# Kernel optimization log

Measured on AMD Instinct MI355X. Metric: run time of the kernel, lower is better.

Reference implementation:

```python
import jax, jax.numpy as jnp
import numpy as np

N, E, G = 10000, 160000, 64
F, C1, C2, C3, K, NC = 128, 128, 256, 512, 5, 10


def setup_inputs() -> dict:
    key = jax.random.key(0)
    ks = jax.random.split(key, 12)
    s = 0.05
    return {
        "x": jax.random.normal(ks[0], (N, F), dtype=jnp.float32),
        "edge_index": jax.random.randint(ks[1], (2, E), 0, N, dtype=jnp.int64),
        "batch": jnp.sort(jax.random.randint(ks[2], (N,), 0, G, dtype=jnp.int64)),
        "W_cheb": jax.random.normal(ks[3], (K, F, C1), dtype=jnp.float32) * s,
        "b_cheb": jnp.zeros((C1,), jnp.float32),
        "W_g1": jax.random.normal(ks[4], (C1, C2), dtype=jnp.float32) * s,
        "b_g1": jnp.zeros((C2,), jnp.float32),
        "W_g2": jax.random.normal(ks[5], (C2, C3), dtype=jnp.float32) * s,
        "b_g2": jnp.zeros((C3,), jnp.float32),
        "w_gate": jax.random.normal(ks[6], (C3, 1), dtype=jnp.float32) * s,
        "b_gate": jnp.zeros((1,), jnp.float32),
        "W_fc": jax.random.normal(ks[7], (C3, NC), dtype=jnp.float32) * s,
        "b_fc": jnp.zeros((NC,), jnp.float32),
    }


def _deg_inv_sqrt(deg):
    return jnp.where(deg > 0, jax.lax.rsqrt(jnp.maximum(deg, 1e-12)), 0.0)


def cheb_conv(x, src, dst, W, b):
    # PyG ChebConv, sym normalization, lambda_max=2 => scaled Laplacian = -D^-1/2 A D^-1/2
    ones = jnp.ones((src.shape[0],), x.dtype)
    deg = jax.ops.segment_sum(ones, src, num_segments=N)
    dinv = _deg_inv_sqrt(deg)
    w = -(dinv[src] * dinv[dst])  # [E]

    def prop(h):
        return jax.ops.segment_sum(w[:, None] * h[src], dst, num_segments=N)

    tx0 = x
    tx1 = prop(x)
    out = tx0 @ W[0] + tx1 @ W[1]
    for k in range(2, W.shape[0]):
        tx2 = 2.0 * prop(tx1) - tx0
        out = out + tx2 @ W[k]
        tx0, tx1 = tx1, tx2
    return out + b


def gcn_conv(x, src, dst, W, b):
    # PyG GCNConv: add self-loops, sym norm D~^-1/2 (A+I) D~^-1/2, transform then aggregate
    loop = jnp.arange(N, dtype=src.dtype)
    src_a = jnp.concatenate([src, loop])
    dst_a = jnp.concatenate([dst, loop])
    ones = jnp.ones((src_a.shape[0],), x.dtype)
    deg = jax.ops.segment_sum(ones, dst_a, num_segments=N)
    dinv = _deg_inv_sqrt(deg)
    norm = dinv[src_a] * dinv[dst_a]  # [E+N]
    h = x @ W
    return jax.ops.segment_sum(norm[:, None] * h[src_a], dst_a, num_segments=N) + b


def attention_pool(x, batch, w_gate, b_gate):
    logits = (x @ w_gate + b_gate)[:, 0]  # [N]
    m = jax.ops.segment_max(logits, batch, num_segments=G)
    e = jnp.exp(logits - m[batch])
    s = jax.ops.segment_sum(e, batch, num_segments=G)
    alpha = e / s[batch]
    return jax.ops.segment_sum(alpha[:, None] * x, batch, num_segments=G)  # [G, C3]


def reference(x, edge_index, batch, W_cheb, b_cheb, W_g1, b_g1, W_g2, b_g2,
              w_gate, b_gate, W_fc, b_fc):
    src, dst = edge_index[0], edge_index[1]
    h = jax.nn.relu(cheb_conv(x, src, dst, W_cheb, b_cheb))
    h = jax.nn.relu(gcn_conv(h, src, dst, W_g1, b_g1))
    h = jax.nn.relu(gcn_conv(h, src, dst, W_g2, b_g2))
    g = attention_pool(h, batch, w_gate, b_gate)
    logits = g @ W_fc + b_fc
    return jax.nn.log_softmax(logits, axis=1)
```

## Files before the change

### kernel.cpp

```cpp
#include <hip/hip_runtime.h>
#include <hip/hip_bf16.h>
#include <math.h>

#define N_NODES 10000
#define N_EDGES 160000
#define N_GRAPHS 64
#define F_IN    128
#define C1_DIM  128
#define C2_DIM  256
#define C3_DIM  512
#define K_CHEB  5
#define NCLS    10
#define TC      (K_CHEB * F_IN)

typedef short v8s __attribute__((ext_vector_type(8)));
typedef float v4f __attribute__((ext_vector_type(4)));

static __device__ __forceinline__ unsigned short f2bf(float f) {
    unsigned u = __float_as_uint(f);
    unsigned r = (u + 0x7FFFu + ((u >> 16) & 1u)) >> 16;
    return (unsigned short)r;
}
static __device__ __forceinline__ float bf_lo(unsigned u) { return __uint_as_float(u << 16); }
static __device__ __forceinline__ float bf_hi(unsigned u) { return __uint_as_float(u & 0xFFFF0000u); }

#define PREP_A (N_NODES * 32)
#define PREP_B (TC * C1_DIM)
#define PREP_C (C1_DIM * C2_DIM)
#define PREP_D (C2_DIM * C3_DIM)
#define PREP_E N_NODES
#define PREP_F N_NODES
#define PREP_H (N_GRAPHS * C3_DIM)
#define PREP_G N_EDGES
#define PREP_TOTAL (PREP_A + PREP_B + PREP_C + PREP_D + PREP_E + PREP_F + PREP_H + PREP_G)
__global__ void prep_kernel(const float* __restrict__ x, unsigned short* __restrict__ tcat,
                            const float* __restrict__ Wcheb, unsigned short* __restrict__ Wcb_t,
                            const float* __restrict__ Wg1, unsigned short* __restrict__ Wg1_t,
                            const float* __restrict__ Wg2, unsigned short* __restrict__ Wg2_t,
                            const int* __restrict__ batch, int* __restrict__ gptr,
                            float* __restrict__ logits, float* __restrict__ pooled,
                            const int* __restrict__ src, const int* __restrict__ dst,
                            int* __restrict__ cnt_s, int* __restrict__ cnt_d) {
    int id = blockIdx.x * blockDim.x + threadIdx.x;
    if (id < PREP_A) {
        int n = id >> 5, f = (id & 31) * 4;
        float4 v = *(const float4*)(x + (size_t)n * F_IN + f);
        ushort4 o; o.x = f2bf(v.x); o.y = f2bf(v.y); o.z = f2bf(v.z); o.w = f2bf(v.w);
        *(ushort4*)(tcat + (size_t)n * TC + f) = o;
        return;
    }
    id -= PREP_A;
    if (id < PREP_B) {
        int k = id % TC, n = id / TC;
        Wcb_t[(size_t)n * TC + k] = f2bf(Wcheb[(size_t)k * C1_DIM + n]);
        return;
    }
    id -= PREP_B;
    if (id < PREP_C) {
        int k = id % C1_DIM, n = id / C1_DIM;
        Wg1_t[(size_t)n * C1_DIM + k] = f2bf(Wg1[(size_t)k * C2_DIM + n]);
        return;
    }
    id -= PREP_C;
    if (id < PREP_D) {
        int k = id % C2_DIM, n = id / C2_DIM;
        Wg2_t[(size_t)n * C2_DIM + k] = f2bf(Wg2[(size_t)k * C3_DIM + n]);
        return;
    }
    id -= PREP_D;
    if (id < PREP_E) {
        int i = id;
        int b = batch[i];
        if (i == 0) { for (int g = 0; g <= b; g++) gptr[g] = 0; }
        else {
            int bp = batch[i - 1];
            for (int g = bp + 1; g <= b; g++) gptr[g] = i;
        }
        if (i == N_NODES - 1) { for (int g = b + 1; g <= N_GRAPHS; g++) gptr[g] = N_NODES; }
        return;
    }
    id -= PREP_E;
    if (id < PREP_F) { logits[id] = 0.0f; return; }
    id -= PREP_F;
    if (id < PREP_H) { pooled[id] = 0.0f; return; }
    id -= PREP_H;
    if (id < PREP_G) {
        atomicAdd(&cnt_s[src[id]], 1);
        atomicAdd(&cnt_d[dst[id]], 1);
    }
}

__global__ __launch_bounds__(256) void fill_scan_kernel(
        const int* __restrict__ src, const int* __restrict__ dst,
        const int* __restrict__ cnt_s, const int* __restrict__ cnt_d,
        int* __restrict__ rowptr, int* __restrict__ fillc,
        int2* __restrict__ ecb, int2* __restrict__ egc, int E, int n) {
    __shared__ int ldsc[N_NODES];
    __shared__ int sums[256];
    int tid = threadIdx.x;
    for (int i = tid; i < n; i += 256) ldsc[i] = cnt_d[i];
    __syncthreads();
    int chunk = (n + 255) / 256;
    int s0 = min(n, tid * chunk), s1 = min(n, s0 + chunk);
    int loc = 0;
    for (int i = s0; i < s1; i++) loc += ldsc[i];
    sums[tid] = loc;
    __syncthreads();
    for (int off = 1; off < 256; off <<= 1) {
        int t = (tid >= off) ? sums[tid - off] : 0;
        __syncthreads();
        sums[tid] += t;
        __syncthreads();
    }
    int pre = sums[tid] - loc;
    for (int i = s0; i < s1; i++) { int v = ldsc[i]; ldsc[i] = pre; pre += v; }
    __syncthreads();
    if (blockIdx.x == 0) {
        for (int i = tid; i < n; i += 256) rowptr[i] = ldsc[i];
        if (tid == 255) rowptr[n] = pre;
    }
    int e = blockIdx.x * 256 + tid;
    if (e >= E) return;
    int s = src[e], d = dst[e];
    int pos = ldsc[d] + atomicAdd(&fillc[d], 1);
    int cs = cnt_s[s], cd = cnt_s[d];
    float ds = (cs > 0) ? rsqrtf((float)cs) : 0.0f;
    float dd = (cd > 0) ? rsqrtf((float)cd) : 0.0f;
    float nr = rsqrtf((float)cnt_d[s] + 1.0f) * rsqrtf((float)cnt_d[d] + 1.0f);
    ecb[pos] = make_int2(s, __float_as_int(-(ds * dd)));
    egc[pos] = make_int2(s, __float_as_int(nr));
}

__global__ __launch_bounds__(256) void gather_cheb_bf(
        const unsigned short* __restrict__ tb, const int* __restrict__ rowptr,
        const int2* __restrict__ edges,
        const unsigned short* __restrict__ base, float alpha, float beta,
        unsigned short* __restrict__ outc, int n) {
    int w = (blockIdx.x * blockDim.x + threadIdx.x) >> 6;
    int lane = threadIdx.x & 63;
    if (w >= n) return;
    w = __builtin_amdgcn_readfirstlane(w);
    int rs = __builtin_amdgcn_readfirstlane(rowptr[w]);
    int re = __builtin_amdgcn_readfirstlane(rowptr[w + 1]);
    float a0 = 0.0f, a1 = 0.0f;
    for (int b = rs; b < re; b += 64) {
        int nv = min(64, re - b);
        int cl = 0, wlb = 0;
        if (b + lane < re) { int2 e = edges[b + lane]; cl = e.x; wlb = e.y; }
        int nk = (nv + 15) & ~15;
        for (int j = 0; j < nk; j += 16) {
            int ss[16]; float ww[16]; unsigned uu[16];
            #pragma unroll
            for (int q = 0; q < 16; q++) {
                ss[q] = __builtin_amdgcn_readlane(cl, j + q);
                ww[q] = __uint_as_float((unsigned)__builtin_amdgcn_readlane(wlb, j + q));
            }
            #pragma unroll
            for (int q = 0; q < 16; q++)
                uu[q] = *(const unsigned*)(tb + (size_t)ss[q] * TC + lane * 2);
            #pragma unroll
            for (int q = 0; q < 16; q++) { a0 += ww[q] * bf_lo(uu[q]); a1 += ww[q] * bf_hi(uu[q]); }
        }
    }
    if (base) {
        unsigned ub = ((const unsigned*)(base + (size_t)w * TC))[lane];
        a0 = alpha * a0 + beta * bf_lo(ub);
        a1 = alpha * a1 + beta * bf_hi(ub);
    } else {
        a0 *= alpha; a1 *= alpha;
    }
    ushort2 o; o.x = f2bf(a0); o.y = f2bf(a1);
    *(ushort2*)(outc + (size_t)w * TC + lane * 2) = o;
}

template<int FPL>
__global__ __launch_bounds__(256) void gather_gcn_pre(
        const unsigned short* __restrict__ tb, const int* __restrict__ rowptr,
        const int2* __restrict__ edges,
        const int* __restrict__ cnt_d, unsigned short* __restrict__ z, int n) {
    const int C = FPL * 64;
    int w = (blockIdx.x * blockDim.x + threadIdx.x) >> 6;
    int lane = threadIdx.x & 63;
    if (w >= n) return;
    w = __builtin_amdgcn_readfirstlane(w);
    int rs = __builtin_amdgcn_readfirstlane(rowptr[w]);
    int re = __builtin_amdgcn_readfirstlane(rowptr[w + 1]);
    float acc[FPL];
    #pragma unroll
    for (int q = 0; q < FPL; q++) acc[q] = 0.0f;
    for (int b = rs; b < re; b += 64) {
        int nv = min(64, re - b);
        int cl = 0, wlb = 0;
        if (b + lane < re) { int2 e = edges[b + lane]; cl = e.x; wlb = e.y; }
        int nk = (nv + 15) & ~15;
        for (int j = 0; j < nk; j += 16) {
            int ss[16]; float ww[16];
            #pragma unroll
            for (int q = 0; q < 16; q++) {
                ss[q] = __builtin_amdgcn_readlane(cl, j + q);
                ww[q] = __uint_as_float((unsigned)__builtin_amdgcn_readlane(wlb, j + q));
            }
            if constexpr (FPL == 2) {
                unsigned uu[16];
                #pragma unroll
                for (int q = 0; q < 16; q++)
                    uu[q] = *(const unsigned*)(tb + (size_t)ss[q] * C + lane * 2);
                #pragma unroll
                for (int q = 0; q < 16; q++) { acc[0] += ww[q] * bf_lo(uu[q]); acc[1] += ww[q] * bf_hi(uu[q]); }
            } else {
                uint2 uu[16];
                #pragma unroll
                for (int q = 0; q < 16; q++)
                    uu[q] = *(const uint2*)(tb + (size_t)ss[q] * C + lane * 4);
                #pragma unroll
                for (int q = 0; q < 16; q++) {
                    acc[0] += ww[q] * bf_lo(uu[q].x); acc[1] += ww[q] * bf_hi(uu[q].x);
                    acc[2] += ww[q] * bf_lo(uu[q].y); acc[3] += ww[q] * bf_hi(uu[q].y);
                }
            }
        }
    }
    float sn = 1.0f / (float)(cnt_d[w] + 1);
    if constexpr (FPL == 2) {
        unsigned u = ((const unsigned*)(tb + (size_t)w * C))[lane];
        acc[0] += sn * bf_lo(u); acc[1] += sn * bf_hi(u);
        ushort2 o; o.x = f2bf(acc[0]); o.y = f2bf(acc[1]);
        *(ushort2*)(z + (size_t)w * C + lane * 2) = o;
    } else {
        uint2 u = ((const uint2*)(tb + (size_t)w * C))[lane];
        acc[0] += sn * bf_lo(u.x); acc[1] += sn * bf_hi(u.x);
        acc[2] += sn * bf_lo(u.y); acc[3] += sn * bf_hi(u.y);
        ushort4 o; o.x = f2bf(acc[0]); o.y = f2bf(acc[1]);
        o.z = f2bf(acc[2]); o.w = f2bf(acc[3]);
        *(ushort4*)(z + (size_t)w * C + lane * 4) = o;
    }
}

template<int JT, int KC>
__global__ __launch_bounds__(256) void gemm_bf16(
        const unsigned short* __restrict__ A, const unsigned short* __restrict__ Bt,
        const float* __restrict__ bias,
        unsigned short* __restrict__ Cb, const float* __restrict__ wg,
        float* __restrict__ logits, int M, int N) {
    int m0 = blockIdx.y * 64, n0 = blockIdx.x * (JT * 32);
    int wave = threadIdx.x >> 6, lane = threadIdx.x & 63;
    int wm = (wave & 1) * 32, wn = (wave >> 1) * (JT * 16);
    int l15 = lane & 15, quad = lane >> 4;

    v4f acc[2][JT];
    #pragma unroll
    for (int i = 0; i < 2; i++)
        #pragma unroll
        for (int j = 0; j < JT; j++) acc[i][j] = (v4f){0.f, 0.f, 0.f, 0.f};

    const unsigned short* Ab[2]; bool av[2];
    #pragma unroll
    for (int i = 0; i < 2; i++) {
        int row = m0 + wm + i * 16 + l15;
        av[i] = row < M;
        Ab[i] = A + (size_t)(av[i] ? row : 0) * KC + quad * 8;
    }
    const unsigned short* Bb[JT];
    #pragma unroll
    for (int j = 0; j < JT; j++) {
        int coln = n0 + wn + j * 16 + l15;
        Bb[j] = Bt + (size_t)coln * KC + quad * 8;
    }
    const v8s zero8 = {0, 0, 0, 0, 0, 0, 0, 0};

    #pragma unroll
    for (int k0 = 0; k0 < KC; k0 += 32) {
        v8s a[2], b[JT];
        #pragma unroll
        for (int i = 0; i < 2; i++) a[i] = av[i] ? *(const v8s*)(Ab[i] + k0) : zero8;
        #pragma unroll
        for (int j = 0; j < JT; j++) b[j] = *(const v8s*)(Bb[j] + k0);
        #pragma unroll
        for (int i = 0; i < 2; i++)
            #pragma unroll
            for (int j = 0; j < JT; j++)
                acc[i][j] = __builtin_amdgcn_mfma_f32_16x16x32_bf16(a[i], b[j], acc[i][j], 0, 0, 0);
    }

    float bv[JT], wgj[JT];
    #pragma unroll
    for (int j = 0; j < JT; j++) {
        int coln = n0 + wn + j * 16 + l15;
        bv[j] = bias[coln];
        wgj[j] = wg ? wg[coln] : 0.0f;
    }
    #pragma unroll
    for (int i = 0; i < 2; i++) {
        #pragma unroll
        for (int r = 0; r < 4; r++) {
            int row = m0 + wm + i * 16 + quad * 4 + r;
            if (row >= M) continue;
            float gval = 0.0f;
            #pragma unroll
            for (int j = 0; j < JT; j++) {
                int coln = n0 + wn + j * 16 + l15;
                float v = fmaxf(acc[i][j][r] + bv[j], 0.0f);
                Cb[(size_t)row * N + coln] = f2bf(v);
                gval += v * wgj[j];
            }
            if (wg) {
                #pragma unroll
                for (int off = 1; off < 16; off <<= 1) gval += __shfl_xor(gval, off);
                if (l15 == 0) atomicAdd(&logits[row], gval);
            }
        }
    }
}

__global__ __launch_bounds__(256) void pool_partial(const unsigned short* __restrict__ h3b,
        const float* __restrict__ logits, const int* __restrict__ gptr,
        float* __restrict__ pooled) {
    __shared__ float red[256];
    int g = blockIdx.x, sl = blockIdx.y, tid = threadIdx.x;
    int gs = gptr[g], ge = gptr[g + 1];
    float m = -INFINITY;
    for (int i = gs + tid; i < ge; i += 256) m = fmaxf(m, logits[i]);
    red[tid] = m; __syncthreads();
    for (int off = 128; off > 0; off >>= 1) {
        if (tid < off) red[tid] = fmaxf(red[tid], red[tid + off]);
        __syncthreads();
    }
    m = red[0]; __syncthreads();
    float s = 0.0f;
    for (int i = gs + tid; i < ge; i += 256) s += expf(logits[i] - m);
    red[tid] = s; __syncthreads();
    for (int off = 128; off > 0; off >>= 1) {
        if (tid < off) red[tid] += red[tid + off];
        __syncthreads();
    }
    s = red[0];
    float sinv = (s > 0.0f) ? 1.0f / s : 0.0f;
    int cnt = ge - gs;
    int i0 = gs + (cnt * sl) / 8;
    int i1 = gs + (cnt * (sl + 1)) / 8;
    float a0 = 0.0f, a1 = 0.0f;
    for (int i = i0; i < i1; i++) {
        float al = expf(logits[i] - m) * sinv;
        unsigned u = ((const unsigned*)(h3b + (size_t)i * C3_DIM))[tid];
        a0 += al * bf_lo(u);
        a1 += al * bf_hi(u);
    }
    if (i1 > i0) {
        atomicAdd(&pooled[(size_t)g * C3_DIM + tid * 2 + 0], a0);
        atomicAdd(&pooled[(size_t)g * C3_DIM + tid * 2 + 1], a1);
    }
}

__global__ void fc_kernel(const float* __restrict__ pooled, const float* __restrict__ Wfc,
                          const float* __restrict__ bfc, float* __restrict__ out) {
    int g = blockIdx.x;
    int t = threadIdx.x;
    float acc = -INFINITY;
    if (t < NCLS) {
        acc = bfc[t];
        for (int k = 0; k < C3_DIM; k++)
            acc += pooled[(size_t)g * C3_DIM + k] * Wfc[k * NCLS + t];
    }
    float m = acc;
    #pragma unroll
    for (int off = 8; off > 0; off >>= 1) m = fmaxf(m, __shfl_xor(m, off, 16));
    float e = (t < NCLS) ? expf(acc - m) : 0.0f;
    float s = e;
    #pragma unroll
    for (int off = 8; off > 0; off >>= 1) s += __shfl_xor(s, off, 16);
    if (t < NCLS) out[g * NCLS + t] = acc - m - logf(s);
}

extern "C" void kernel_launch(void* const* d_in, const int* in_sizes, int n_in,
                              void* d_out, int out_size, void* d_ws, size_t ws_size,
                              hipStream_t stream) {
    const float* x      = (const float*)d_in[0];
    const int*   ei     = (const int*)d_in[1];
    const int*   batch  = (const int*)d_in[2];
    const float* W_cheb = (const float*)d_in[3];
    const float* b_cheb = (const float*)d_in[4];
    const float* W_g1   = (const float*)d_in[5];
    const float* b_g1   = (const float*)d_in[6];
    const float* W_g2   = (const float*)d_in[7];
    const float* b_g2   = (const float*)d_in[8];
    const float* w_gate = (const float*)d_in[9];
    const float* W_fc   = (const float*)d_in[11];
    const float* b_fc   = (const float*)d_in[12];
    const int* src = ei;
    const int* dst = ei + N_EDGES;
    float* out = (float*)d_out;

    const int N = N_NODES, E = N_EDGES, G = N_GRAPHS;

    char* Wp = (char*)d_ws;
    auto alloc = [&](size_t bytes) {
        void* p = Wp;
        Wp += (bytes + 255) & ~(size_t)255;
        return p;
    };
    int*   cnt3    = (int*)alloc((size_t)3 * N * 4);
    int*   cnt_s   = cnt3;
    int*   cnt_d   = cnt3 + N;
    int*   fillc   = cnt3 + 2 * N;
    int*   rowptr  = (int*)alloc((N + 1) * 4);
    int2*  ecb     = (int2*)alloc((size_t)E * 8);
    int2*  egc     = (int2*)alloc((size_t)E * 8);
    unsigned short* tcat  = (unsigned short*)alloc((size_t)N * TC * 2);
    unsigned short* h1b   = (unsigned short*)alloc((size_t)N * C1_DIM * 2);
    unsigned short* z1b   = (unsigned short*)alloc((size_t)N * C1_DIM * 2);
    unsigned short* h2b   = (unsigned short*)alloc((size_t)N * C2_DIM * 2);
    unsigned short* z2b   = (unsigned short*)alloc((size_t)N * C2_DIM * 2);
    unsigned short* h3b   = (unsigned short*)alloc((size_t)N * C3_DIM * 2);
    unsigned short* Wcb_t = (unsigned short*)alloc((size_t)TC * C1_DIM * 2);
    unsigned short* Wg1_t = (unsigned short*)alloc((size_t)C1_DIM * C2_DIM * 2);
    unsigned short* Wg2_t = (unsigned short*)alloc((size_t)C2_DIM * C3_DIM * 2);
    float* logits  = (float*)alloc(N * 4);
    int*   gptr    = (int*)alloc((G + 1) * 4);
    float* pooled  = (float*)alloc((size_t)G * C3_DIM * 4);

    dim3 blk(256);
    auto cdiv = [](int a, int b) { return (a + b - 1) / b; };

    hipMemsetAsync(cnt3, 0, (size_t)3 * N * sizeof(int), stream);
    hipLaunchKernelGGL(prep_kernel, dim3(cdiv(PREP_TOTAL, 256)), blk, 0, stream,
                       x, tcat, W_cheb, Wcb_t, W_g1, Wg1_t, W_g2, Wg2_t,
                       batch, gptr, logits, pooled, src, dst, cnt_s, cnt_d);

    hipLaunchKernelGGL(fill_scan_kernel, dim3(cdiv(E, 256)), blk, 0, stream,
                       src, dst, cnt_s, cnt_d, rowptr, fillc, ecb, egc, E, N);

    const int NWB = cdiv(N, 4);

    hipLaunchKernelGGL(gather_cheb_bf, dim3(NWB), blk, 0, stream,
                       tcat + 0 * F_IN, rowptr, ecb,
                       (const unsigned short*)nullptr, 1.0f, 0.0f, tcat + 1 * F_IN, N);
    hipLaunchKernelGGL(gather_cheb_bf, dim3(NWB), blk, 0, stream,
                       tcat + 1 * F_IN, rowptr, ecb,
                       tcat + 0 * F_IN, 2.0f, -1.0f, tcat + 2 * F_IN, N);
    hipLaunchKernelGGL(gather_cheb_bf, dim3(NWB), blk, 0, stream,
                       tcat + 2 * F_IN, rowptr, ecb,
                       tcat + 1 * F_IN, 2.0f, -1.0f, tcat + 3 * F_IN, N);
    hipLaunchKernelGGL(gather_cheb_bf, dim3(NWB), blk, 0, stream,
                       tcat + 3 * F_IN, rowptr, ecb,
                       tcat + 2 * F_IN, 2.0f, -1.0f, tcat + 4 * F_IN, N);

    hipLaunchKernelGGL((gemm_bf16<2, TC>), dim3(C1_DIM / 64, cdiv(N, 64)), blk, 0, stream,
                       tcat, Wcb_t, b_cheb, h1b,
                       (const float*)nullptr, (float*)nullptr, N, C1_DIM);

    hipLaunchKernelGGL(gather_gcn_pre<2>, dim3(NWB), blk, 0, stream,
                       h1b, rowptr, egc, cnt_d, z1b, N);
    hipLaunchKernelGGL((gemm_bf16<4, C1_DIM>), dim3(C2_DIM / 128, cdiv(N, 64)), blk, 0, stream,
                       z1b, Wg1_t, b_g1, h2b,
                       (const float*)nullptr, (float*)nullptr, N, C2_DIM);

    hipLaunchKernelGGL(gather_gcn_pre<4>, dim3(NWB), blk, 0, stream,
                       h2b, rowptr, egc, cnt_d, z2b, N);
    hipLaunchKernelGGL((gemm_bf16<4, C2_DIM>), dim3(C3_DIM / 128, cdiv(N, 64)), blk, 0, stream,
                       z2b, Wg2_t, b_g2, h3b,
                       w_gate, logits, N, C3_DIM);

    hipLaunchKernelGGL(pool_partial, dim3(G, 8), blk, 0, stream, h3b, logits, gptr, pooled);
    hipLaunchKernelGGL(fc_kernel, dim3(G), dim3(64), 0, stream, pooled, W_fc, b_fc, out);
}
```

Before: 259.7 us.

## Fuse gather, GEMM, pool and FC stages into one cooperative persistent kernel

Replaces the ten separate stage kernels (four Chebyshev gathers, three GEMMs, two GCN gathers, pool, FC) with a single cooperative mega-kernel. The grid is sized from occupancy and capped at 1024 blocks, each stage uses grid-stride loops, and grid.sync() separates the stages. The aim is to remove per-launch overhead and inter-kernel gaps. In exchange it adds grid-wide barriers, caps parallelism to resident blocks, and may raise register pressure because all stage code lives in one kernel.

```diff
diff --git a/kernel.cpp b/kernel.cpp
--- a/kernel.cpp
+++ b/kernel.cpp
@@ -1,6 +1,9 @@
 #include <hip/hip_runtime.h>
+#include <hip/hip_cooperative_groups.h>
 #include <hip/hip_bf16.h>
 #include <math.h>
+
+namespace cg = cooperative_groups;
 
 #define N_NODES 10000
 #define N_EDGES 160000
@@ -131,244 +134,303 @@
     egc[pos] = make_int2(s, __float_as_int(nr));
 }
 
-__global__ __launch_bounds__(256) void gather_cheb_bf(
+static __device__ void dev_gather_cheb(
         const unsigned short* __restrict__ tb, const int* __restrict__ rowptr,
         const int2* __restrict__ edges,
         const unsigned short* __restrict__ base, float alpha, float beta,
-        unsigned short* __restrict__ outc, int n) {
-    int w = (blockIdx.x * blockDim.x + threadIdx.x) >> 6;
-    int lane = threadIdx.x & 63;
-    if (w >= n) return;
-    w = __builtin_amdgcn_readfirstlane(w);
-    int rs = __builtin_amdgcn_readfirstlane(rowptr[w]);
-    int re = __builtin_amdgcn_readfirstlane(rowptr[w + 1]);
-    float a0 = 0.0f, a1 = 0.0f;
-    for (int b = rs; b < re; b += 64) {
-        int nv = min(64, re - b);
-        int cl = 0, wlb = 0;
-        if (b + lane < re) { int2 e = edges[b + lane]; cl = e.x; wlb = e.y; }
-        int nk = (nv + 15) & ~15;
-        for (int j = 0; j < nk; j += 16) {
-            int ss[16]; float ww[16]; unsigned uu[16];
-            #pragma unroll
-            for (int q = 0; q < 16; q++) {
-                ss[q] = __builtin_amdgcn_readlane(cl, j + q);
-                ww[q] = __uint_as_float((unsigned)__builtin_amdgcn_readlane(wlb, j + q));
+        unsigned short* __restrict__ outc, int n, int wave0, int nwaves, int lane) {
+    for (int w0 = wave0; w0 < n; w0 += nwaves) {
+        int w = __builtin_amdgcn_readfirstlane(w0);
+        int rs = __builtin_amdgcn_readfirstlane(rowptr[w]);
+        int re = __builtin_amdgcn_readfirstlane(rowptr[w + 1]);
+        float a0 = 0.0f, a1 = 0.0f;
+        for (int b = rs; b < re; b += 64) {
+            int nv = min(64, re - b);
+            int cl = 0, wlb = 0;
+            if (b + lane < re) { int2 e = edges[b + lane]; cl = e.x; wlb = e.y; }
+            int nk = (nv + 15) & ~15;
+            for (int j = 0; j < nk; j += 16) {
+                int ss[16]; float ww[16]; unsigned uu[16];
+                #pragma unroll
+                for (int q = 0; q < 16; q++) {
+                    ss[q] = __builtin_amdgcn_readlane(cl, j + q);
+                    ww[q] = __uint_as_float((unsigned)__builtin_amdgcn_readlane(wlb, j + q));
+                }
+                #pragma unroll
+                for (int q = 0; q < 16; q++)
+                    uu[q] = *(const unsigned*)(tb + (size_t)ss[q] * TC + lane * 2);
+                #pragma unroll
+                for (int q = 0; q < 16; q++) { a0 += ww[q] * bf_lo(uu[q]); a1 += ww[q] * bf_hi(uu[q]); }
             }
-            #pragma unroll
-            for (int q = 0; q < 16; q++)
-                uu[q] = *(const unsigned*)(tb + (size_t)ss[q] * TC + lane * 2);
-            #pragma unroll
-            for (int q = 0; q < 16; q++) { a0 += ww[q] * bf_lo(uu[q]); a1 += ww[q] * bf_hi(uu[q]); }
-        }
-    }
-    if (base) {
-        unsigned ub = ((const unsigned*)(base + (size_t)w * TC))[lane];
-        a0 = alpha * a0 + beta * bf_lo(ub);
-        a1 = alpha * a1 + beta * bf_hi(ub);
-    } else {
-        a0 *= alpha; a1 *= alpha;
-    }
-    ushort2 o; o.x = f2bf(a0); o.y = f2bf(a1);
-    *(ushort2*)(outc + (size_t)w * TC + lane * 2) = o;
+        }
+        if (base) {
+            unsigned ub = ((const unsigned*)(base + (size_t)w * TC))[lane];
+            a0 = alpha * a0 + beta * bf_lo(ub);
+            a1 = alpha * a1 + beta * bf_hi(ub);
+        } else {
+            a0 *= alpha; a1 *= alpha;
+        }
+        ushort2 o; o.x = f2bf(a0); o.y = f2bf(a1);
+        *(ushort2*)(outc + (size_t)w * TC + lane * 2) = o;
+    }
 }
 
 template<int FPL>
-__global__ __launch_bounds__(256) void gather_gcn_pre(
+static __device__ void dev_gather_gcn(
         const unsigned short* __restrict__ tb, const int* __restrict__ rowptr,
         const int2* __restrict__ edges,
-        const int* __restrict__ cnt_d, unsigned short* __restrict__ z, int n) {
+        const int* __restrict__ cnt_d, unsigned short* __restrict__ z, int n,
+        int wave0, int nwaves, int lane) {
     const int C = FPL * 64;
-    int w = (blockIdx.x * blockDim.x + threadIdx.x) >> 6;
-    int lane = threadIdx.x & 63;
-    if (w >= n) return;
-    w = __builtin_amdgcn_readfirstlane(w);
-    int rs = __builtin_amdgcn_readfirstlane(rowptr[w]);
-    int re = __builtin_amdgcn_readfirstlane(rowptr[w + 1]);
-    float acc[FPL];
-    #pragma unroll
-    for (int q = 0; q < FPL; q++) acc[q] = 0.0f;
-    for (int b = rs; b < re; b += 64) {
-        int nv = min(64, re - b);
-        int cl = 0, wlb = 0;
-        if (b + lane < re) { int2 e = edges[b + lane]; cl = e.x; wlb = e.y; }
-        int nk = (nv + 15) & ~15;
-        for (int j = 0; j < nk; j += 16) {
-            int ss[16]; float ww[16];
-            #pragma unroll
-            for (int q = 0; q < 16; q++) {
-                ss[q] = __builtin_amdgcn_readlane(cl, j + q);
-                ww[q] = __uint_as_float((unsigned)__builtin_amdgcn_readlane(wlb, j + q));
-            }
-            if constexpr (FPL == 2) {
-                unsigned uu[16];
-                #pragma unroll
-                for (int q = 0; q < 16; q++)
-                    uu[q] = *(const unsigned*)(tb + (size_t)ss[q] * C + lane * 2);
-                #pragma unroll
-                for (int q = 0; q < 16; q++) { acc[0] += ww[q] * bf_lo(uu[q]); acc[1] += ww[q] * bf_hi(uu[q]); }
-            } else {
-                uint2 uu[16];
-                #pragma unroll
-                for (int q = 0; q < 16; q++)
-                    uu[q] = *(const uint2*)(tb + (size_t)ss[q] * C + lane * 4);
+    for (int w0 = wave0; w0 < n; w0 += nwaves) {
+        int w = __builtin_amdgcn_readfirstlane(w0);
+        int rs = __builtin_amdgcn_readfirstlane(rowptr[w]);
+        int re = __builtin_amdgcn_readfirstlane(rowptr[w + 1]);
+        float acc[FPL];
+        #pragma unroll
+        for (int q = 0; q < FPL; q++) acc[q] = 0.0f;
+        for (int b = rs; b < re; b += 64) {
+            int nv = min(64, re - b);
+            int cl = 0, wlb = 0;
+            if (b + lane < re) { int2 e = edges[b + lane]; cl = e.x; wlb = e.y; }
+            int nk = (nv + 15) & ~15;
+            for (int j = 0; j < nk; j += 16) {
+                int ss[16]; float ww[16];
                 #pragma unroll
                 for (int q = 0; q < 16; q++) {
-                    acc[0] += ww[q] * bf_lo(uu[q].x); acc[1] += ww[q] * bf_hi(uu[q].x);
-                    acc[2] += ww[q] * bf_lo(uu[q].y); acc[3] += ww[q] * bf_hi(uu[q].y);
+                    ss[q] = __builtin_amdgcn_readlane(cl, j + q);
+                    ww[q] = __uint_as_float((unsigned)__builtin_amdgcn_readlane(wlb, j + q));
+                }
+                if constexpr (FPL == 2) {
+                    unsigned uu[16];
+                    #pragma unroll
+                    for (int q = 0; q < 16; q++)
+                        uu[q] = *(const unsigned*)(tb + (size_t)ss[q] * C + lane * 2);
+                    #pragma unroll
+                    for (int q = 0; q < 16; q++) { acc[0] += ww[q] * bf_lo(uu[q]); acc[1] += ww[q] * bf_hi(uu[q]); }
+                } else {
+                    uint2 uu[16];
+                    #pragma unroll
+                    for (int q = 0; q < 16; q++)
+                        uu[q] = *(const uint2*)(tb + (size_t)ss[q] * C + lane * 4);
+                    #pragma unroll
+                    for (int q = 0; q < 16; q++) {
+                        acc[0] += ww[q] * bf_lo(uu[q].x); acc[1] += ww[q] * bf_hi(uu[q].x);
+                        acc[2] += ww[q] * bf_lo(uu[q].y); acc[3] += ww[q] * bf_hi(uu[q].y);
+                    }
                 }
             }
         }
-    }
-    float sn = 1.0f / (float)(cnt_d[w] + 1);
-    if constexpr (FPL == 2) {
-        unsigned u = ((const unsigned*)(tb + (size_t)w * C))[lane];
-        acc[0] += sn * bf_lo(u); acc[1] += sn * bf_hi(u);
-        ushort2 o; o.x = f2bf(acc[0]); o.y = f2bf(acc[1]);
-        *(ushort2*)(z + (size_t)w * C + lane * 2) = o;
-    } else {
-        uint2 u = ((const uint2*)(tb + (size_t)w * C))[lane];
-        acc[0] += sn * bf_lo(u.x); acc[1] += sn * bf_hi(u.x);
-        acc[2] += sn * bf_lo(u.y); acc[3] += sn * bf_hi(u.y);
-        ushort4 o; o.x = f2bf(acc[0]); o.y = f2bf(acc[1]);
-        o.z = f2bf(acc[2]); o.w = f2bf(acc[3]);
-        *(ushort4*)(z + (size_t)w * C + lane * 4) = o;
+        float sn = 1.0f / (float)(cnt_d[w] + 1);
+        if constexpr (FPL == 2) {
+            unsigned u = ((const unsigned*)(tb + (size_t)w * C))[lane];
+            acc[0] += sn * bf_lo(u); acc[1] += sn * bf_hi(u);
+            ushort2 o; o.x = f2bf(acc[0]); o.y = f2bf(acc[1]);
+            *(ushort2*)(z + (size_t)w * C + lane * 2) = o;
+        } else {
+            uint2 u = ((const uint2*)(tb + (size_t)w * C))[lane];
+            acc[0] += sn * bf_lo(u.x); acc[1] += sn * bf_hi(u.x);
+            acc[2] += sn * bf_lo(u.y); acc[3] += sn * bf_hi(u.y);
+            ushort4 o; o.x = f2bf(acc[0]); o.y = f2bf(acc[1]);
+            o.z = f2bf(acc[2]); o.w = f2bf(acc[3]);
+            *(ushort4*)(z + (size_t)w * C + lane * 4) = o;
+        }
     }
 }
 
 template<int JT, int KC>
-__global__ __launch_bounds__(256) void gemm_bf16(
+static __device__ void dev_gemm(
         const unsigned short* __restrict__ A, const unsigned short* __restrict__ Bt,
         const float* __restrict__ bias,
         unsigned short* __restrict__ Cb, const float* __restrict__ wg,
-        float* __restrict__ logits, int M, int N) {
-    int m0 = blockIdx.y * 64, n0 = blockIdx.x * (JT * 32);
+        float* __restrict__ logits, int M, int N, int bid, int nb) {
+    const int nx = N / (JT * 32);
+    const int ntiles = nx * ((M + 63) >> 6);
     int wave = threadIdx.x >> 6, lane = threadIdx.x & 63;
     int wm = (wave & 1) * 32, wn = (wave >> 1) * (JT * 16);
     int l15 = lane & 15, quad = lane >> 4;
-
-    v4f acc[2][JT];
-    #pragma unroll
-    for (int i = 0; i < 2; i++)
-        #pragma unroll
-        for (int j = 0; j < JT; j++) acc[i][j] = (v4f){0.f, 0.f, 0.f, 0.f};
-
-    const unsigned short* Ab[2]; bool av[2];
-    #pragma unroll
-    for (int i = 0; i < 2; i++) {
-        int row = m0 + wm + i * 16 + l15;
-        av[i] = row < M;
-        Ab[i] = A + (size_t)(av[i] ? row : 0) * KC + quad * 8;
-    }
-    const unsigned short* Bb[JT];
-    #pragma unroll
-    for (int j = 0; j < JT; j++) {
-        int coln = n0 + wn + j * 16 + l15;
-        Bb[j] = Bt + (size_t)coln * KC + quad * 8;
-    }
     const v8s zero8 = {0, 0, 0, 0, 0, 0, 0, 0};
 
-    #pragma unroll
-    for (int k0 = 0; k0 < KC; k0 += 32) {
-        v8s a[2], b[JT];
-        #pragma unroll
-        for (int i = 0; i < 2; i++) a[i] = av[i] ? *(const v8s*)(Ab[i] + k0) : zero8;
-        #pragma unroll
-        for (int j = 0; j < JT; j++) b[j] = *(const v8s*)(Bb[j] + k0);
+    for (int t = bid; t < ntiles; t += nb) {
+        int m0 = (t / nx) * 64, n0 = (t % nx) * (JT * 32);
+
+        v4f acc[2][JT];
         #pragma unroll
         for (int i = 0; i < 2; i++)
             #pragma unroll
-            for (int j = 0; j < JT; j++)
-                acc[i][j] = __builtin_amdgcn_mfma_f32_16x16x32_bf16(a[i], b[j], acc[i][j], 0, 0, 0);
-    }
-
-    float bv[JT], wgj[JT];
-    #pragma unroll
-    for (int j = 0; j < JT; j++) {
-        int coln = n0 + wn + j * 16 + l15;
-        bv[j] = bias[coln];
-        wgj[j] = wg ? wg[coln] : 0.0f;
-    }
-    #pragma unroll
-    for (int i = 0; i < 2; i++) {
-        #pragma unroll
-        for (int r = 0; r < 4; r++) {
-            int row = m0 + wm + i * 16 + quad * 4 + r;
-            if (row >= M) continue;
-            float gval = 0.0f;
-            #pragma unroll
-            for (int j = 0; j < JT; j++) {
-                int coln = n0 + wn + j * 16 + l15;
-                float v = fmaxf(acc[i][j][r] + bv[j], 0.0f);
-                Cb[(size_t)row * N + coln] = f2bf(v);
-                gval += v * wgj[j];
+            for (int j = 0; j < JT; j++) acc[i][j] = (v4f){0.f, 0.f, 0.f, 0.f};
+
+        const unsigned short* Ab[2]; bool av[2];
+        #pragma unroll
+        for (int i = 0; i < 2; i++) {
+            int row = m0 + wm + i * 16 + l15;
+            av[i] = row < M;
+            Ab[i] = A + (size_t)(av[i] ? row : 0) * KC + quad * 8;
+        }
+        const unsigned short* Bb[JT];
+        #pragma unroll
+        for (int j = 0; j < JT; j++) {
+            int coln = n0 + wn + j * 16 + l15;
+            Bb[j] = Bt + (size_t)coln * KC + quad * 8;
+        }
+
+        #pragma unroll
+        for (int k0 = 0; k0 < KC; k0 += 32) {
+            v8s a[2], b[JT];
+            #pragma unroll
+            for (int i = 0; i < 2; i++) a[i] = av[i] ? *(const v8s*)(Ab[i] + k0) : zero8;
+            #pragma unroll
+            for (int j = 0; j < JT; j++) b[j] = *(const v8s*)(Bb[j] + k0);
+            #pragma unroll
+            for (int i = 0; i < 2; i++)
+                #pragma unroll
+                for (int j = 0; j < JT; j++)
+                    acc[i][j] = __builtin_amdgcn_mfma_f32_16x16x32_bf16(a[i], b[j], acc[i][j], 0, 0, 0);
+        }
+
+        float bv[JT], wgj[JT];
+        #pragma unroll
+        for (int j = 0; j < JT; j++) {
+            int coln = n0 + wn + j * 16 + l15;
+            bv[j] = bias[coln];
+            wgj[j] = wg ? wg[coln] : 0.0f;
+        }
+        #pragma unroll
+        for (int i = 0; i < 2; i++) {
+            #pragma unroll
+            for (int r = 0; r < 4; r++) {
+                int row = m0 + wm + i * 16 + quad * 4 + r;
+                if (row >= M) continue;
+                float gval = 0.0f;
+                #pragma unroll
+                for (int j = 0; j < JT; j++) {
+                    int coln = n0 + wn + j * 16 + l15;
+                    float v = fmaxf(acc[i][j][r] + bv[j], 0.0f);
+                    Cb[(size_t)row * N + coln] = f2bf(v);
+                    gval += v * wgj[j];
+                }
+                if (wg) {
+                    #pragma unroll
+                    for (int off = 1; off < 16; off <<= 1) gval += __shfl_xor(gval, off);
+                    if (l15 == 0) atomicAdd(&logits[row], gval);
+                }
             }
-            if (wg) {
-                #pragma unroll
-                for (int off = 1; off < 16; off <<= 1) gval += __shfl_xor(gval, off);
-                if (l15 == 0) atomicAdd(&logits[row], gval);
+        }
+    }
+}
+
+static __device__ void dev_pool(const unsigned short* __restrict__ h3b,
+        const float* __restrict__ logits, const int* __restrict__ gptr,
+        float* __restrict__ pooled, int bid, int nb) {
+    __shared__ float red[256];
+    int tid = threadIdx.x;
+    for (int vb = bid; vb < N_GRAPHS * 8; vb += nb) {
+        int g = vb >> 3, sl = vb & 7;
+        int gs = gptr[g], ge = gptr[g + 1];
+        float m = -INFINITY;
+        for (int i = gs + tid; i < ge; i += 256) m = fmaxf(m, logits[i]);
+        red[tid] = m; __syncthreads();
+        for (int off = 128; off > 0; off >>= 1) {
+            if (tid < off) red[tid] = fmaxf(red[tid], red[tid + off]);
+            __syncthreads();
+        }
+        m = red[0]; __syncthreads();
+        float s = 0.0f;
+        for (int i = gs + tid; i < ge; i += 256) s += expf(logits[i] - m);
+        red[tid] = s; __syncthreads();
+        for (int off = 128; off > 0; off >>= 1) {
+            if (tid < off) red[tid] += red[tid + off];
+            __syncthreads();
+        }
+        s = red[0]; __syncthreads();
+        float sinv = (s > 0.0f) ? 1.0f / s : 0.0f;
+        int cnt = ge - gs;
+        int i0 = gs + (cnt * sl) / 8;
+        int i1 = gs + (cnt * (sl + 1)) / 8;
+        float a0 = 0.0f, a1 = 0.0f;
+        for (int i = i0; i < i1; i++) {
+            float al = expf(logits[i] - m) * sinv;
+            unsigned u = ((const unsigned*)(h3b + (size_t)i * C3_DIM))[tid];
+            a0 += al * bf_lo(u);
+            a1 += al * bf_hi(u);
+        }
+        if (i1 > i0) {
+            atomicAdd(&pooled[(size_t)g * C3_DIM + tid * 2 + 0], a0);
+            atomicAdd(&pooled[(size_t)g * C3_DIM + tid * 2 + 1], a1);
+        }
+    }
+}
+
+static __device__ void dev_fc(const float* __restrict__ pooled, const float* __restrict__ Wfc,
+                              const float* __restrict__ bfc, float* __restrict__ out,
+                              int bid, int nb) {
+    int t = threadIdx.x;
+    for (int g = bid; g < N_GRAPHS; g += nb) {
+        if (t < 64) {
+            float acc = -INFINITY;
+            if (t < NCLS) {
+                acc = bfc[t];
+                for (int k = 0; k < C3_DIM; k++)
+                    acc += pooled[(size_t)g * C3_DIM + k] * Wfc[k * NCLS + t];
             }
-        }
-    }
-}
-
-__global__ __launch_bounds__(256) void pool_partial(const unsigned short* __restrict__ h3b,
-        const float* __restrict__ logits, const int* __restrict__ gptr,
-        float* __restrict__ pooled) {
-    __shared__ float red[256];
-    int g = blockIdx.x, sl = blockIdx.y, tid = threadIdx.x;
-    int gs = gptr[g], ge = gptr[g + 1];
-    float m = -INFINITY;
-    for (int i = gs + tid; i < ge; i += 256) m = fmaxf(m, logits[i]);
-    red[tid] = m; __syncthreads();
-    for (int off = 128; off > 0; off >>= 1) {
-        if (tid < off) red[tid] = fmaxf(red[tid], red[tid + off]);
-        __syncthreads();
-    }
-    m = red[0]; __syncthreads();
-    float s = 0.0f;
-    for (int i = gs + tid; i < ge; i += 256) s += expf(logits[i] - m);
-    red[tid] = s; __syncthreads();
-    for (int off = 128; off > 0; off >>= 1) {
-        if (tid < off) red[tid] += red[tid + off];
-        __syncthreads();
-    }
-    s = red[0];
-    float sinv = (s > 0.0f) ? 1.0f / s : 0.0f;
-    int cnt = ge - gs;
-    int i0 = gs + (cnt * sl) / 8;
-    int i1 = gs + (cnt * (sl + 1)) / 8;
-    float a0 = 0.0f, a1 = 0.0f;
-    for (int i = i0; i < i1; i++) {
-        float al = expf(logits[i] - m) * sinv;
-        unsigned u = ((const unsigned*)(h3b + (size_t)i * C3_DIM))[tid];
-        a0 += al * bf_lo(u);
-        a1 += al * bf_hi(u);
-    }
-    if (i1 > i0) {
-        atomicAdd(&pooled[(size_t)g * C3_DIM + tid * 2 + 0], a0);
-        atomicAdd(&pooled[(size_t)g * C3_DIM + tid * 2 + 1], a1);
-    }
-}
-
-__global__ void fc_kernel(const float* __restrict__ pooled, const float* __restrict__ Wfc,
-                          const float* __restrict__ bfc, float* __restrict__ out) {
-    int g = blockIdx.x;
-    int t = threadIdx.x;
-    float acc = -INFINITY;
-    if (t < NCLS) {
-        acc = bfc[t];
-        for (int k = 0; k < C3_DIM; k++)
-            acc += pooled[(size_t)g * C3_DIM + k] * Wfc[k * NCLS + t];
-    }
-    float m = acc;
-    #pragma unroll
-    for (int off = 8; off > 0; off >>= 1) m = fmaxf(m, __shfl_xor(m, off, 16));
-    float e = (t < NCLS) ? expf(acc - m) : 0.0f;
-    float s = e;
-    #pragma unroll
-    for (int off = 8; off > 0; off >>= 1) s += __shfl_xor(s, off, 16);
-    if (t < NCLS) out[g * NCLS + t] = acc - m - logf(s);
+            float m = acc;
+            #pragma unroll
+            for (int off = 8; off > 0; off >>= 1) m = fmaxf(m, __shfl_xor(m, off, 16));
+            float e = (t < NCLS) ? expf(acc - m) : 0.0f;
+            float s = e;
+            #pragma unroll
+            for (int off = 8; off > 0; off >>= 1) s += __shfl_xor(s, off, 16);
+            if (t < NCLS) out[g * NCLS + t] = acc - m - logf(s);
+        }
+    }
+}
+
+__global__ __launch_bounds__(256, 4) void mega_kernel(
+        unsigned short* tcat, const int* rowptr, const int2* ecb, const int2* egc,
+        const int* cnt_d,
+        const unsigned short* Wcb_t, const float* b_cheb, unsigned short* h1b,
+        unsigned short* z1b, const unsigned short* Wg1_t, const float* b_g1, unsigned short* h2b,
+        unsigned short* z2b, const unsigned short* Wg2_t, const float* b_g2, unsigned short* h3b,
+        const float* w_gate, float* logits, const int* gptr, float* pooled,
+        const float* W_fc, const float* b_fc, float* out) {
+    cg::grid_group grid = cg::this_grid();
+    const int bid = blockIdx.x, nb = gridDim.x;
+    const int lane = threadIdx.x & 63;
+    const int wave0 = bid * 4 + (threadIdx.x >> 6);
+    const int nwaves = nb * 4;
+
+    dev_gather_cheb(tcat + 0 * F_IN, rowptr, ecb, (const unsigned short*)nullptr,
+                    1.0f, 0.0f, tcat + 1 * F_IN, N_NODES, wave0, nwaves, lane);
+    grid.sync();
+    dev_gather_cheb(tcat + 1 * F_IN, rowptr, ecb, tcat + 0 * F_IN,
+                    2.0f, -1.0f, tcat + 2 * F_IN, N_NODES, wave0, nwaves, lane);
+    grid.sync();
+    dev_gather_cheb(tcat + 2 * F_IN, rowptr, ecb, tcat + 1 * F_IN,
+                    2.0f, -1.0f, tcat + 3 * F_IN, N_NODES, wave0, nwaves, lane);
+    grid.sync();
+    dev_gather_cheb(tcat + 3 * F_IN, rowptr, ecb, tcat + 2 * F_IN,
+                    2.0f, -1.0f, tcat + 4 * F_IN, N_NODES, wave0, nwaves, lane);
+    grid.sync();
+
+    dev_gemm<2, TC>(tcat, Wcb_t, b_cheb, h1b, (const float*)nullptr, (float*)nullptr,
+                    N_NODES, C1_DIM, bid, nb);
+    grid.sync();
+
+    dev_gather_gcn<2>(h1b, rowptr, egc, cnt_d, z1b, N_NODES, wave0, nwaves, lane);
+    grid.sync();
+    dev_gemm<4, C1_DIM>(z1b, Wg1_t, b_g1, h2b, (const float*)nullptr, (float*)nullptr,
+                        N_NODES, C2_DIM, bid, nb);
+    grid.sync();
+
+    dev_gather_gcn<4>(h2b, rowptr, egc, cnt_d, z2b, N_NODES, wave0, nwaves, lane);
+    grid.sync();
+    dev_gemm<4, C2_DIM>(z2b, Wg2_t, b_g2, h3b, w_gate, logits, N_NODES, C3_DIM, bid, nb);
+    grid.sync();
+
+    dev_pool(h3b, logits, gptr, pooled, bid, nb);
+    grid.sync();
+
+    dev_fc(pooled, W_fc, b_fc, out, bid, nb);
 }
 
 extern "C" void kernel_launch(void* const* d_in, const int* in_sizes, int n_in,
@@ -429,37 +491,19 @@
     hipLaunchKernelGGL(fill_scan_kernel, dim3(cdiv(E, 256)), blk, 0, stream,
                        src, dst, cnt_s, cnt_d, rowptr, fillc, ecb, egc, E, N);
 
-    const int NWB = cdiv(N, 4);
-
-    hipLaunchKernelGGL(gather_cheb_bf, dim3(NWB), blk, 0, stream,
-                       tcat + 0 * F_IN, rowptr, ecb,
-                       (const unsigned short*)nullptr, 1.0f, 0.0f, tcat + 1 * F_IN, N);
-    hipLaunchKernelGGL(gather_cheb_bf, dim3(NWB), blk, 0, stream,
-                       tcat + 1 * F_IN, rowptr, ecb,
-                       tcat + 0 * F_IN, 2.0f, -1.0f, tcat + 2 * F_IN, N);
-    hipLaunchKernelGGL(gather_cheb_bf, dim3(NWB), blk, 0, stream,
-                       tcat + 2 * F_IN, rowptr, ecb,
-                       tcat + 1 * F_IN, 2.0f, -1.0f, tcat + 3 * F_IN, N);
-    hipLaunchKernelGGL(gather_cheb_bf, dim3(NWB), blk, 0, stream,
-                       tcat + 3 * F_IN, rowptr, ecb,
-                       tcat + 2 * F_IN, 2.0f, -1.0f, tcat + 4 * F_IN, N);
-
-    hipLaunchKernelGGL((gemm_bf16<2, TC>), dim3(C1_DIM / 64, cdiv(N, 64)), blk, 0, stream,
-                       tcat, Wcb_t, b_cheb, h1b,
-                       (const float*)nullptr, (float*)nullptr, N, C1_DIM);
-
-    hipLaunchKernelGGL(gather_gcn_pre<2>, dim3(NWB), blk, 0, stream,
-                       h1b, rowptr, egc, cnt_d, z1b, N);
-    hipLaunchKernelGGL((gemm_bf16<4, C1_DIM>), dim3(C2_DIM / 128, cdiv(N, 64)), blk, 0, stream,
-                       z1b, Wg1_t, b_g1, h2b,
-                       (const float*)nullptr, (float*)nullptr, N, C2_DIM);
-
-    hipLaunchKernelGGL(gather_gcn_pre<4>, dim3(NWB), blk, 0, stream,
-                       h2b, rowptr, egc, cnt_d, z2b, N);
-    hipLaunchKernelGGL((gemm_bf16<4, C2_DIM>), dim3(C3_DIM / 128, cdiv(N, 64)), blk, 0, stream,
-                       z2b, Wg2_t, b_g2, h3b,
-                       w_gate, logits, N, C3_DIM);
-
-    hipLaunchKernelGGL(pool_partial, dim3(G, 8), blk, 0, stream, h3b, logits, gptr, pooled);
-    hipLaunchKernelGGL(fc_kernel, dim3(G), dim3(64), 0, stream, pooled, W_fc, b_fc, out);
-}
+    static int s_gb = 0;
+    if (s_gb == 0) {
+        int bpc = 0;
+        if (hipOccupancyMaxActiveBlocksPerMultiprocessor(&bpc, mega_kernel, 256, 0)
+                != hipSuccess || bpc < 1) bpc = 2;
+        long cap = (long)bpc * 256;
+        s_gb = (int)(cap < 1024 ? cap : 1024);
+    }
+    void* args[] = { &tcat, &rowptr, &ecb, &egc, &cnt_d,
+                     &Wcb_t, &b_cheb, &h1b,
+                     &z1b, &Wg1_t, &b_g1, &h2b,
+                     &z2b, &Wg2_t, &b_g2, &h3b,
+                     &w_gate, &logits, &gptr, &pooled,
+                     &W_fc, &b_fc, &out };
+    hipLaunchCooperativeKernel((void*)mega_kernel, dim3(s_gb), blk, args, 0, stream);
+}
```

Result: slower. 863.5 us (+232.5%).
